# Kernel tuning notes

Measured on AMD Instinct MI355X. Metric: run time of the kernel, lower is better.

## Reference

```python
import jax, jax.numpy as jnp
import numpy as np

N_NODES = 8192


def spmm(edge_src, edge_dst, edge_w, h):
    # out[dst] += w * h[src]  — sparse adjacency @ dense matrix
    msg = h[edge_src] * edge_w[:, None]
    return jax.ops.segment_sum(msg, edge_dst, num_segments=N_NODES)


def setup_inputs() -> dict:
    key = jax.random.key(0)
    k_x, k_s, k_d, k_w, k_w1, k_w2 = jax.random.split(key, 6)
    x = jax.random.normal(k_x, (N_NODES, 512), dtype=jnp.float32)
    edge_src = jax.random.randint(k_s, (262144,), 0, N_NODES, dtype=jnp.int32)
    edge_dst = jax.random.randint(k_d, (262144,), 0, N_NODES, dtype=jnp.int32)
    edge_w = jax.random.uniform(k_w, (262144,), dtype=jnp.float32)
    W1 = jax.random.normal(k_w1, (512, 256), dtype=jnp.float32) * 0.05
    W2 = jax.random.normal(k_w2, (256, 64), dtype=jnp.float32) * 0.05
    return {"x": x, "edge_src": edge_src, "edge_dst": edge_dst,
            "edge_w": edge_w, "W1": W1, "W2": W2}


def reference(x, edge_src, edge_dst, edge_w, W1, W2):
    # GCN layer 1: relu(A @ (X W1))
    h1 = jax.nn.relu(spmm(edge_src, edge_dst, edge_w, x @ W1))
    # GCN layer 2 (linear act): Z = A @ (H1 W2)
    z = spmm(edge_src, edge_dst, edge_w, h1 @ W2)
    # InnerProductDecoder with identity act: Z @ Z^T
    recon = jnp.einsum('nd,md->nm', z, z)
    return recon
```

## Files before the change

kernel.cpp:

```cpp
#include <hip/hip_runtime.h>
#include <hip/hip_bf16.h>

#define NN     8192
#define D0     512
#define D1     256
#define D2     64
#define NE     262144

typedef __attribute__((ext_vector_type(8)))  __bf16 bf16x8;
typedef __attribute__((ext_vector_type(16))) float  f32x16;

__global__ __launch_bounds__(256) void prep_k(const float* __restrict__ W,
                                              int4* __restrict__ zero_region,
                                              __bf16* __restrict__ Th,
                                              __bf16* __restrict__ Tl) {
    const int bid = blockIdx.x;
    const int tid = threadIdx.x;
    if (bid < 16) {
        zero_region[bid * 256 + tid] = make_int4(0, 0, 0, 0);
    } else {
        __shared__ float t[32][33];
        const int cid = bid - 16;
        const int c0 = (cid & 7) * 32;
        const int k0 = (cid >> 3) * 32;
        {
            int tr  = tid >> 3;
            int tc4 = tid & 7;
            float4 v = *reinterpret_cast<const float4*>(&W[(k0 + tr) * D1 + c0 + tc4 * 4]);
            t[tr][tc4 * 4 + 0] = v.x;
            t[tr][tc4 * 4 + 1] = v.y;
            t[tr][tc4 * 4 + 2] = v.z;
            t[tr][tc4 * 4 + 3] = v.w;
        }
        __syncthreads();
        int c  = tid >> 3;
        int kq = (tid & 7) * 4;
        __bf16 hv[4], lv[4];
        #pragma unroll
        for (int j = 0; j < 4; ++j) {
            float f = t[kq + j][c];
            hv[j] = (__bf16)f;
            lv[j] = (__bf16)(f - (float)hv[j]);
        }
        *reinterpret_cast<uint2*>(&Th[(size_t)(c0 + c) * D0 + k0 + kq]) = *reinterpret_cast<uint2*>(hv);
        *reinterpret_cast<uint2*>(&Tl[(size_t)(c0 + c) * D0 + k0 + kq]) = *reinterpret_cast<uint2*>(lv);
    }
}

__global__ __launch_bounds__(256) void gemm1hist_k(const float* __restrict__ X,
                                                   const __bf16* __restrict__ Wh,
                                                   const __bf16* __restrict__ Wl,
                                                   float* __restrict__ O,
                                                   const int4* __restrict__ dst4,
                                                   int* __restrict__ counts) {
    const int gid = blockIdx.x;
    const int tid = threadIdx.x;
    if (gid >= 128) {
        int i = (gid - 128) * 256 + tid;
        int4 d = dst4[i];
        atomicAdd(&counts[d.x], 1);
        atomicAdd(&counts[d.y], 1);
        atomicAdd(&counts[d.z], 1);
        atomicAdd(&counts[d.w], 1);
        return;
    }
    const int bx = gid >> 1;
    const int by = gid & 1;
    const int lane = tid & 63;
    const int w    = tid >> 6;
    const int wm   = w >> 1;
    const int wn   = w & 1;
    const int r32  = lane & 31;
    const int kh   = lane >> 5;
    const int rowBase = bx * 128 + wm * 64;
    const int colBase = by * 128 + wn * 64;

    f32x16 acc[2][2] = {};

    for (int k0 = 0; k0 < D0; k0 += 16) {
        const int koff = k0 + kh * 8;
        bf16x8 ah[2], al[2];
        #pragma unroll
        for (int i = 0; i < 2; ++i) {
            const float* px = X + (size_t)(rowBase + i * 32 + r32) * D0 + koff;
            float4 f0 = *reinterpret_cast<const float4*>(px);
            float4 f1 = *reinterpret_cast<const float4*>(px + 4);
            float f[8] = {f0.x, f0.y, f0.z, f0.w, f1.x, f1.y, f1.z, f1.w};
            #pragma unroll
            for (int e = 0; e < 8; ++e) {
                __bf16 hj = (__bf16)f[e];
                ah[i][e] = hj;
                al[i][e] = (__bf16)(f[e] - (float)hj);
            }
        }
        bf16x8 bh[2], bl[2];
        #pragma unroll
        for (int j = 0; j < 2; ++j) {
            bh[j] = *reinterpret_cast<const bf16x8*>(Wh + (size_t)(colBase + j * 32 + r32) * D0 + koff);
            bl[j] = *reinterpret_cast<const bf16x8*>(Wl + (size_t)(colBase + j * 32 + r32) * D0 + koff);
        }
        #pragma unroll
        for (int i = 0; i < 2; ++i)
            #pragma unroll
            for (int j = 0; j < 2; ++j) {
                acc[i][j] = __builtin_amdgcn_mfma_f32_32x32x16_bf16(ah[i], bh[j], acc[i][j], 0, 0, 0);
                acc[i][j] = __builtin_amdgcn_mfma_f32_32x32x16_bf16(ah[i], bl[j], acc[i][j], 0, 0, 0);
                acc[i][j] = __builtin_amdgcn_mfma_f32_32x32x16_bf16(al[i], bh[j], acc[i][j], 0, 0, 0);
            }
    }

    #pragma unroll
    for (int i = 0; i < 2; ++i)
        #pragma unroll
        for (int j = 0; j < 2; ++j)
            #pragma unroll
            for (int reg = 0; reg < 16; ++reg) {
                int r = (reg & 3) + 8 * (reg >> 2) + 4 * kh;
                O[(size_t)(rowBase + i * 32 + r) * D1 + colBase + j * 32 + r32] = acc[i][j][reg];
            }
}

__global__ __launch_bounds__(256) void scan_k(const int* __restrict__ counts,
                                              int* __restrict__ rs) {
    __shared__ int wsum[4];
    const int tid  = threadIdx.x;
    const int base = tid * 32;
    int v[32];
    int s = 0;
    #pragma unroll
    for (int j = 0; j < 8; ++j) {
        int4 q = reinterpret_cast<const int4*>(&counts[base])[j];
        v[j * 4 + 0] = q.x; v[j * 4 + 1] = q.y; v[j * 4 + 2] = q.z; v[j * 4 + 3] = q.w;
        s += q.x + q.y + q.z + q.w;
    }
    int inc = s;
    #pragma unroll
    for (int off = 1; off < 64; off <<= 1) {
        int t = __shfl_up(inc, off, 64);
        if ((tid & 63) >= off) inc += t;
    }
    if ((tid & 63) == 63) wsum[tid >> 6] = inc;
    __syncthreads();
    int wpre = 0;
    #pragma unroll
    for (int wi = 0; wi < 4; ++wi) if (wi < (tid >> 6)) wpre += wsum[wi];
    int ex = wpre + inc - s;
    #pragma unroll
    for (int j = 0; j < 32; ++j) { rs[base + j] = ex; ex += v[j]; }
    if (tid == 0) rs[NN] = NE;
}

__global__ __launch_bounds__(256) void scatter_k(const int4* __restrict__ src4,
                                                 const int4* __restrict__ dst4,
                                                 const float4* __restrict__ w4,
                                                 const int* __restrict__ rs,
                                                 int* __restrict__ cursor,
                                                 int* __restrict__ eps,
                                                 float* __restrict__ epw) {
    int i = blockIdx.x * 256 + threadIdx.x;
    int4   s = src4[i];
    int4   d = dst4[i];
    float4 w = w4[i];
    int p;
    p = rs[d.x] + atomicAdd(&cursor[d.x], 1); eps[p] = s.x; epw[p] = w.x;
    p = rs[d.y] + atomicAdd(&cursor[d.y], 1); eps[p] = s.y; epw[p] = w.y;
    p = rs[d.z] + atomicAdd(&cursor[d.z], 1); eps[p] = s.z; epw[p] = w.z;
    p = rs[d.w] + atomicAdd(&cursor[d.w], 1); eps[p] = s.w; epw[p] = w.w;
}

__global__ __launch_bounds__(256) void spmmfuse_k(const float* __restrict__ Hin,
                                                  const int* __restrict__ rs,
                                                  const int* __restrict__ eps,
                                                  const float* __restrict__ epw,
                                                  const float* __restrict__ W2,
                                                  float* __restrict__ H1W2) {
    __shared__ float h1row[4][D1];
    const int tid = threadIdx.x;
    const int g   = tid >> 6;
    const int lc  = (tid & 63) * 4;
    const int row = blockIdx.x * 4 + g;
    const int start = rs[row], end = rs[row + 1];
    float4 acc = make_float4(0.f, 0.f, 0.f, 0.f);
    for (int j = start; j < end; ++j) {
        const float w = epw[j];
        float4 v = *reinterpret_cast<const float4*>(&Hin[(size_t)eps[j] * D1 + lc]);
        acc.x += w * v.x; acc.y += w * v.y; acc.z += w * v.z; acc.w += w * v.w;
    }
    h1row[g][lc + 0] = fmaxf(acc.x, 0.f);
    h1row[g][lc + 1] = fmaxf(acc.y, 0.f);
    h1row[g][lc + 2] = fmaxf(acc.z, 0.f);
    h1row[g][lc + 3] = fmaxf(acc.w, 0.f);
    __syncthreads();
    const int c = tid & 63;
    float o = 0.f;
    #pragma unroll 16
    for (int k = 0; k < D1; ++k) o += h1row[g][k] * W2[k * D2 + c];
    H1W2[(size_t)row * D2 + c] = o;
}

__global__ __launch_bounds__(256) void spmm64_k(const float* __restrict__ Hin,
                                                const int* __restrict__ rs,
                                                const int* __restrict__ eps,
                                                const float* __restrict__ epw,
                                                __bf16* __restrict__ Zh,
                                                __bf16* __restrict__ Zl) {
    const int tid = threadIdx.x;
    const int g   = tid >> 4;
    const int lc  = (tid & 15) * 4;
    const int row = blockIdx.x * 16 + g;
    const int start = rs[row], end = rs[row + 1];
    float4 acc = make_float4(0.f, 0.f, 0.f, 0.f);
    for (int j = start; j < end; ++j) {
        const float w = epw[j];
        float4 v = *reinterpret_cast<const float4*>(&Hin[(size_t)eps[j] * D2 + lc]);
        acc.x += w * v.x; acc.y += w * v.y; acc.z += w * v.z; acc.w += w * v.w;
    }
    float a[4] = {acc.x, acc.y, acc.z, acc.w};
    __bf16 h4[4], l4[4];
    #pragma unroll
    for (int e = 0; e < 4; ++e) {
        __bf16 h = (__bf16)a[e];
        h4[e] = h;
        l4[e] = (__bf16)(a[e] - (float)h);
    }
    *reinterpret_cast<uint2*>(&Zh[(size_t)row * D2 + lc]) = *reinterpret_cast<uint2*>(h4);
    *reinterpret_cast<uint2*>(&Zl[(size_t)row * D2 + lc]) = *reinterpret_cast<uint2*>(l4);
}

__global__ __launch_bounds__(256) void zzt_k(const __bf16* __restrict__ Zh,
                                             const __bf16* __restrict__ Zl,
                                             float* __restrict__ O) {
    const int tid  = threadIdx.x;
    const int lane = tid & 63;
    const int w    = tid >> 6;
    const int wm   = w >> 1;
    const int wn   = w & 1;
    const int r32  = lane & 31;
    const int kh   = lane >> 5;
    const int rowBase = blockIdx.y * 128 + wm * 64;
    const int colBase = blockIdx.x * 128 + wn * 64;

    f32x16 acc[2][2] = {};

    #pragma unroll
    for (int kk = 0; kk < 4; ++kk) {
        const int koff = kk * 16 + kh * 8;
        bf16x8 ah0 = *reinterpret_cast<const bf16x8*>(&Zh[(rowBase +      r32) * D2 + koff]);
        bf16x8 ah1 = *reinterpret_cast<const bf16x8*>(&Zh[(rowBase + 32 + r32) * D2 + koff]);
        bf16x8 al0 = *reinterpret_cast<const bf16x8*>(&Zl[(rowBase +      r32) * D2 + koff]);
        bf16x8 al1 = *reinterpret_cast<const bf16x8*>(&Zl[(rowBase + 32 + r32) * D2 + koff]);
        bf16x8 bh0 = *reinterpret_cast<const bf16x8*>(&Zh[(colBase +      r32) * D2 + koff]);
        bf16x8 bh1 = *reinterpret_cast<const bf16x8*>(&Zh[(colBase + 32 + r32) * D2 + koff]);
        bf16x8 bl0 = *reinterpret_cast<const bf16x8*>(&Zl[(colBase +      r32) * D2 + koff]);
        bf16x8 bl1 = *reinterpret_cast<const bf16x8*>(&Zl[(colBase + 32 + r32) * D2 + koff]);

        acc[0][0] = __builtin_amdgcn_mfma_f32_32x32x16_bf16(ah0, bh0, acc[0][0], 0, 0, 0);
        acc[0][1] = __builtin_amdgcn_mfma_f32_32x32x16_bf16(ah0, bh1, acc[0][1], 0, 0, 0);
        acc[1][0] = __builtin_amdgcn_mfma_f32_32x32x16_bf16(ah1, bh0, acc[1][0], 0, 0, 0);
        acc[1][1] = __builtin_amdgcn_mfma_f32_32x32x16_bf16(ah1, bh1, acc[1][1], 0, 0, 0);

        acc[0][0] = __builtin_amdgcn_mfma_f32_32x32x16_bf16(ah0, bl0, acc[0][0], 0, 0, 0);
        acc[0][1] = __builtin_amdgcn_mfma_f32_32x32x16_bf16(ah0, bl1, acc[0][1], 0, 0, 0);
        acc[1][0] = __builtin_amdgcn_mfma_f32_32x32x16_bf16(ah1, bl0, acc[1][0], 0, 0, 0);
        acc[1][1] = __builtin_amdgcn_mfma_f32_32x32x16_bf16(ah1, bl1, acc[1][1], 0, 0, 0);

        acc[0][0] = __builtin_amdgcn_mfma_f32_32x32x16_bf16(al0, bh0, acc[0][0], 0, 0, 0);
        acc[0][1] = __builtin_amdgcn_mfma_f32_32x32x16_bf16(al0, bh1, acc[0][1], 0, 0, 0);
        acc[1][0] = __builtin_amdgcn_mfma_f32_32x32x16_bf16(al1, bh0, acc[1][0], 0, 0, 0);
        acc[1][1] = __builtin_amdgcn_mfma_f32_32x32x16_bf16(al1, bh1, acc[1][1], 0, 0, 0);
    }

    #pragma unroll
    for (int i = 0; i < 2; ++i)
        #pragma unroll
        for (int j = 0; j < 2; ++j)
            #pragma unroll
            for (int reg = 0; reg < 16; ++reg) {
                int r = (reg & 3) + 8 * (reg >> 2) + 4 * kh;
                __builtin_nontemporal_store(acc[i][j][reg],
                    &O[(size_t)(rowBase + i * 32 + r) * NN + colBase + j * 32 + r32]);
            }
}

extern "C" void kernel_launch(void* const* d_in, const int* in_sizes, int n_in,
                              void* d_out, int out_size, void* d_ws, size_t ws_size,
                              hipStream_t stream) {
    const float* x        = (const float*)d_in[0];
    const int*   edge_src = (const int*)d_in[1];
    const int*   edge_dst = (const int*)d_in[2];
    const float* edge_w   = (const float*)d_in[3];
    const float* W1       = (const float*)d_in[4];
    const float* W2       = (const float*)d_in[5];
    float* out = (float*)d_out;

    char* ws = (char*)d_ws;
    const size_t OFF_XW1  = 0;
    const size_t OFF_H1W2 = OFF_XW1  + (size_t)NN * D1 * 4;
    const size_t OFF_ZH   = OFF_H1W2 + (size_t)NN * D2 * 4;
    const size_t OFF_ZL   = OFF_ZH   + (size_t)NN * D2 * 2;
    const size_t OFF_WTH  = OFF_ZL   + (size_t)NN * D2 * 2;
    const size_t OFF_WTL  = OFF_WTH  + (size_t)D0 * D1 * 2;
    const size_t OFF_RS   = OFF_WTL  + (size_t)D0 * D1 * 2;
    const size_t OFF_CNT  = OFF_RS   + 33280;
    const size_t OFF_CUR  = OFF_CNT  + (size_t)NN * 4;
    const size_t OFF_EPS  = OFF_CUR  + (size_t)NN * 4;
    const size_t OFF_EPW  = OFF_EPS  + (size_t)NE * 4;

    float*  xw1  = (float*)(ws + OFF_XW1);
    float*  h1w2 = (float*)(ws + OFF_H1W2);
    __bf16* zh   = (__bf16*)(ws + OFF_ZH);
    __bf16* zl   = (__bf16*)(ws + OFF_ZL);
    __bf16* wth  = (__bf16*)(ws + OFF_WTH);
    __bf16* wtl  = (__bf16*)(ws + OFF_WTL);
    int*    rs   = (int*)(ws + OFF_RS);
    int*    cnt  = (int*)(ws + OFF_CNT);
    int*    cur  = (int*)(ws + OFF_CUR);
    int*    eps  = (int*)(ws + OFF_EPS);
    float*  epw  = (float*)(ws + OFF_EPW);

    prep_k<<<16 + 128, 256, 0, stream>>>(W1, (int4*)cnt, wth, wtl);

    gemm1hist_k<<<128 + 256, 256, 0, stream>>>(x, wth, wtl, xw1,
                                               (const int4*)edge_dst, cnt);

    scan_k<<<1, 256, 0, stream>>>(cnt, rs);
    scatter_k<<<NE / 4 / 256, 256, 0, stream>>>((const int4*)edge_src,
                                                (const int4*)edge_dst,
                                                (const float4*)edge_w,
                                                rs, cur, eps, epw);

    spmmfuse_k<<<NN / 4, 256, 0, stream>>>(xw1, rs, eps, epw, W2, h1w2);

    spmm64_k<<<NN / 16, 256, 0, stream>>>(h1w2, rs, eps, epw, zh, zl);

    zzt_k<<<dim3(NN / 128, NN / 128), 256, 0, stream>>>(zh, zl, out);
}
```

Measured before the change: 211.1 us.

## Shrink GEMM1 tiles, pack edge index/weight pairs, split SpMM1 from GEMM2

GEMM1 now uses 64x64 block tiles with one 32x32 MFMA tile per wave, giving 512 blocks instead of 128 for more parallelism on the GPU. Edge source index and weight are packed into one int2 array so each edge needs one load instead of two. The fused SpMM1+W2 kernel is split into a column-split SpMM kernel (two column halves, 8 rows per block) and a separate small GEMM2 kernel. The split adds an extra pass that writes and reads the full H1 buffer through memory and an additional launch. It also gives up the register-level reuse of X and W tiles that the larger GEMM1 tiles had.

```diff
diff --git a/kernel.cpp b/kernel.cpp
--- a/kernel.cpp
+++ b/kernel.cpp
@@ -55,8 +55,8 @@
                                                    int* __restrict__ counts) {
     const int gid = blockIdx.x;
     const int tid = threadIdx.x;
-    if (gid >= 128) {
-        int i = (gid - 128) * 256 + tid;
+    if (gid >= 512) {
+        int i = (gid - 512) * 256 + tid;
         int4 d = dst4[i];
         atomicAdd(&counts[d.x], 1);
         atomicAdd(&counts[d.y], 1);
@@ -64,60 +64,49 @@
         atomicAdd(&counts[d.w], 1);
         return;
     }
-    const int bx = gid >> 1;
-    const int by = gid & 1;
+    const int bx = gid >> 2;
+    const int by = gid & 3;
     const int lane = tid & 63;
     const int w    = tid >> 6;
     const int wm   = w >> 1;
     const int wn   = w & 1;
     const int r32  = lane & 31;
     const int kh   = lane >> 5;
-    const int rowBase = bx * 128 + wm * 64;
-    const int colBase = by * 128 + wn * 64;
-
-    f32x16 acc[2][2] = {};
-
+    const int row  = bx * 64 + wm * 32 + r32;
+    const int col  = by * 64 + wn * 32 + r32;
+
+    const float*  pX  = X  + (size_t)row * D0;
+    const __bf16* pBh = Wh + (size_t)col * D0;
+    const __bf16* pBl = Wl + (size_t)col * D0;
+
+    f32x16 acc = {};
+    #pragma unroll 4
     for (int k0 = 0; k0 < D0; k0 += 16) {
         const int koff = k0 + kh * 8;
-        bf16x8 ah[2], al[2];
+        float4 f0 = *reinterpret_cast<const float4*>(pX + koff);
+        float4 f1 = *reinterpret_cast<const float4*>(pX + koff + 4);
+        float f[8] = {f0.x, f0.y, f0.z, f0.w, f1.x, f1.y, f1.z, f1.w};
+        bf16x8 ah, al;
         #pragma unroll
-        for (int i = 0; i < 2; ++i) {
-            const float* px = X + (size_t)(rowBase + i * 32 + r32) * D0 + koff;
-            float4 f0 = *reinterpret_cast<const float4*>(px);
-            float4 f1 = *reinterpret_cast<const float4*>(px + 4);
-            float f[8] = {f0.x, f0.y, f0.z, f0.w, f1.x, f1.y, f1.z, f1.w};
-            #pragma unroll
-            for (int e = 0; e < 8; ++e) {
-                __bf16 hj = (__bf16)f[e];
-                ah[i][e] = hj;
-                al[i][e] = (__bf16)(f[e] - (float)hj);
-            }
+        for (int e = 0; e < 8; ++e) {
+            __bf16 hj = (__bf16)f[e];
+            ah[e] = hj;
+            al[e] = (__bf16)(f[e] - (float)hj);
         }
-        bf16x8 bh[2], bl[2];
-        #pragma unroll
-        for (int j = 0; j < 2; ++j) {
-            bh[j] = *reinterpret_cast<const bf16x8*>(Wh + (size_t)(colBase + j * 32 + r32) * D0 + koff);
-            bl[j] = *reinterpret_cast<const bf16x8*>(Wl + (size_t)(colBase + j * 32 + r32) * D0 + koff);
-        }
-        #pragma unroll
-        for (int i = 0; i < 2; ++i)
-            #pragma unroll
-            for (int j = 0; j < 2; ++j) {
-                acc[i][j] = __builtin_amdgcn_mfma_f32_32x32x16_bf16(ah[i], bh[j], acc[i][j], 0, 0, 0);
-                acc[i][j] = __builtin_amdgcn_mfma_f32_32x32x16_bf16(ah[i], bl[j], acc[i][j], 0, 0, 0);
-                acc[i][j] = __builtin_amdgcn_mfma_f32_32x32x16_bf16(al[i], bh[j], acc[i][j], 0, 0, 0);
-            }
-    }
-
-    #pragma unroll
-    for (int i = 0; i < 2; ++i)
-        #pragma unroll
-        for (int j = 0; j < 2; ++j)
-            #pragma unroll
-            for (int reg = 0; reg < 16; ++reg) {
-                int r = (reg & 3) + 8 * (reg >> 2) + 4 * kh;
-                O[(size_t)(rowBase + i * 32 + r) * D1 + colBase + j * 32 + r32] = acc[i][j][reg];
-            }
+        bf16x8 bh = *reinterpret_cast<const bf16x8*>(pBh + koff);
+        bf16x8 bl = *reinterpret_cast<const bf16x8*>(pBl + koff);
+        acc = __builtin_amdgcn_mfma_f32_32x32x16_bf16(ah, bh, acc, 0, 0, 0);
+        acc = __builtin_amdgcn_mfma_f32_32x32x16_bf16(ah, bl, acc, 0, 0, 0);
+        acc = __builtin_amdgcn_mfma_f32_32x32x16_bf16(al, bh, acc, 0, 0, 0);
+    }
+
+    const int rowBase = bx * 64 + wm * 32;
+    const int colBase = by * 64 + wn * 32;
+    #pragma unroll
+    for (int reg = 0; reg < 16; ++reg) {
+        int r = (reg & 3) + 8 * (reg >> 2) + 4 * kh;
+        O[(size_t)(rowBase + r) * D1 + colBase + r32] = acc[reg];
+    }
 }
 
 __global__ __launch_bounds__(256) void scan_k(const int* __restrict__ counts,
@@ -155,53 +144,62 @@
                                                  const float4* __restrict__ w4,
                                                  const int* __restrict__ rs,
                                                  int* __restrict__ cursor,
-                                                 int* __restrict__ eps,
-                                                 float* __restrict__ epw) {
+                                                 int2* __restrict__ ep) {
     int i = blockIdx.x * 256 + threadIdx.x;
     int4   s = src4[i];
     int4   d = dst4[i];
     float4 w = w4[i];
     int p;
-    p = rs[d.x] + atomicAdd(&cursor[d.x], 1); eps[p] = s.x; epw[p] = w.x;
-    p = rs[d.y] + atomicAdd(&cursor[d.y], 1); eps[p] = s.y; epw[p] = w.y;
-    p = rs[d.z] + atomicAdd(&cursor[d.z], 1); eps[p] = s.z; epw[p] = w.z;
-    p = rs[d.w] + atomicAdd(&cursor[d.w], 1); eps[p] = s.w; epw[p] = w.w;
-}
-
-__global__ __launch_bounds__(256) void spmmfuse_k(const float* __restrict__ Hin,
-                                                  const int* __restrict__ rs,
-                                                  const int* __restrict__ eps,
-                                                  const float* __restrict__ epw,
-                                                  const float* __restrict__ W2,
-                                                  float* __restrict__ H1W2) {
-    __shared__ float h1row[4][D1];
-    const int tid = threadIdx.x;
-    const int g   = tid >> 6;
-    const int lc  = (tid & 63) * 4;
-    const int row = blockIdx.x * 4 + g;
+    p = rs[d.x] + atomicAdd(&cursor[d.x], 1); ep[p] = make_int2(s.x, __float_as_int(w.x));
+    p = rs[d.y] + atomicAdd(&cursor[d.y], 1); ep[p] = make_int2(s.y, __float_as_int(w.y));
+    p = rs[d.z] + atomicAdd(&cursor[d.z], 1); ep[p] = make_int2(s.z, __float_as_int(w.z));
+    p = rs[d.w] + atomicAdd(&cursor[d.w], 1); ep[p] = make_int2(s.w, __float_as_int(w.w));
+}
+
+__global__ __launch_bounds__(256) void spmm1_k(const float* __restrict__ Hin,
+                                               const int* __restrict__ rs,
+                                               const int2* __restrict__ ep,
+                                               float* __restrict__ H1) {
+    const int tid = threadIdx.x;
+    const int g   = tid >> 5;
+    const int lc  = blockIdx.y * 128 + (tid & 31) * 4;
+    const int row = blockIdx.x * 8 + g;
     const int start = rs[row], end = rs[row + 1];
     float4 acc = make_float4(0.f, 0.f, 0.f, 0.f);
     for (int j = start; j < end; ++j) {
-        const float w = epw[j];
-        float4 v = *reinterpret_cast<const float4*>(&Hin[(size_t)eps[j] * D1 + lc]);
+        int2 e = ep[j];
+        const float w = __int_as_float(e.y);
+        float4 v = *reinterpret_cast<const float4*>(&Hin[(size_t)e.x * D1 + lc]);
         acc.x += w * v.x; acc.y += w * v.y; acc.z += w * v.z; acc.w += w * v.w;
     }
-    h1row[g][lc + 0] = fmaxf(acc.x, 0.f);
-    h1row[g][lc + 1] = fmaxf(acc.y, 0.f);
-    h1row[g][lc + 2] = fmaxf(acc.z, 0.f);
-    h1row[g][lc + 3] = fmaxf(acc.w, 0.f);
+    float4 r = make_float4(fmaxf(acc.x, 0.f), fmaxf(acc.y, 0.f),
+                           fmaxf(acc.z, 0.f), fmaxf(acc.w, 0.f));
+    *reinterpret_cast<float4*>(&H1[(size_t)row * D1 + lc]) = r;
+}
+
+__global__ __launch_bounds__(256) void gemm2_k(const float* __restrict__ H,
+                                               const float* __restrict__ W,
+                                               float* __restrict__ O) {
+    __shared__ __align__(16) float hs[4][D1];
+    const int tid = threadIdx.x;
+    const int r = tid >> 6;
+    const int c = tid & 63;
+    const int row0 = blockIdx.x * 4;
+    {
+        int lr = tid >> 6, lc4 = tid & 63;
+        *reinterpret_cast<float4*>(&hs[lr][lc4 * 4]) =
+            *reinterpret_cast<const float4*>(&H[(size_t)(row0 + lr) * D1 + lc4 * 4]);
+    }
     __syncthreads();
-    const int c = tid & 63;
-    float o = 0.f;
+    float acc = 0.f;
     #pragma unroll 16
-    for (int k = 0; k < D1; ++k) o += h1row[g][k] * W2[k * D2 + c];
-    H1W2[(size_t)row * D2 + c] = o;
+    for (int k = 0; k < D1; ++k) acc += hs[r][k] * W[k * D2 + c];
+    O[(size_t)(row0 + r) * D2 + c] = acc;
 }
 
 __global__ __launch_bounds__(256) void spmm64_k(const float* __restrict__ Hin,
                                                 const int* __restrict__ rs,
-                                                const int* __restrict__ eps,
-                                                const float* __restrict__ epw,
+                                                const int2* __restrict__ ep,
                                                 __bf16* __restrict__ Zh,
                                                 __bf16* __restrict__ Zl) {
     const int tid = threadIdx.x;
@@ -211,8 +209,9 @@
     const int start = rs[row], end = rs[row + 1];
     float4 acc = make_float4(0.f, 0.f, 0.f, 0.f);
     for (int j = start; j < end; ++j) {
-        const float w = epw[j];
-        float4 v = *reinterpret_cast<const float4*>(&Hin[(size_t)eps[j] * D2 + lc]);
+        int2 e = ep[j];
+        const float w = __int_as_float(e.y);
+        float4 v = *reinterpret_cast<const float4*>(&Hin[(size_t)e.x * D2 + lc]);
         acc.x += w * v.x; acc.y += w * v.y; acc.z += w * v.z; acc.w += w * v.w;
     }
     float a[4] = {acc.x, acc.y, acc.z, acc.w};
@@ -295,7 +294,8 @@
 
     char* ws = (char*)d_ws;
     const size_t OFF_XW1  = 0;
-    const size_t OFF_H1W2 = OFF_XW1  + (size_t)NN * D1 * 4;
+    const size_t OFF_H1   = OFF_XW1  + (size_t)NN * D1 * 4;
+    const size_t OFF_H1W2 = OFF_H1   + (size_t)NN * D1 * 4;
     const size_t OFF_ZH   = OFF_H1W2 + (size_t)NN * D2 * 4;
     const size_t OFF_ZL   = OFF_ZH   + (size_t)NN * D2 * 2;
     const size_t OFF_WTH  = OFF_ZL   + (size_t)NN * D2 * 2;
@@ -303,10 +303,10 @@
     const size_t OFF_RS   = OFF_WTL  + (size_t)D0 * D1 * 2;
     const size_t OFF_CNT  = OFF_RS   + 33280;
     const size_t OFF_CUR  = OFF_CNT  + (size_t)NN * 4;
-    const size_t OFF_EPS  = OFF_CUR  + (size_t)NN * 4;
-    const size_t OFF_EPW  = OFF_EPS  + (size_t)NE * 4;
+    const size_t OFF_EP   = OFF_CUR  + (size_t)NN * 4;
 
     float*  xw1  = (float*)(ws + OFF_XW1);
+    float*  h1   = (float*)(ws + OFF_H1);
     float*  h1w2 = (float*)(ws + OFF_H1W2);
     __bf16* zh   = (__bf16*)(ws + OFF_ZH);
     __bf16* zl   = (__bf16*)(ws + OFF_ZL);
@@ -315,23 +315,24 @@
     int*    rs   = (int*)(ws + OFF_RS);
     int*    cnt  = (int*)(ws + OFF_CNT);
     int*    cur  = (int*)(ws + OFF_CUR);
-    int*    eps  = (int*)(ws + OFF_EPS);
-    float*  epw  = (float*)(ws + OFF_EPW);
+    int2*   ep   = (int2*)(ws + OFF_EP);
 
     prep_k<<<16 + 128, 256, 0, stream>>>(W1, (int4*)cnt, wth, wtl);
 
-    gemm1hist_k<<<128 + 256, 256, 0, stream>>>(x, wth, wtl, xw1,
+    gemm1hist_k<<<512 + 256, 256, 0, stream>>>(x, wth, wtl, xw1,
                                                (const int4*)edge_dst, cnt);
 
     scan_k<<<1, 256, 0, stream>>>(cnt, rs);
     scatter_k<<<NE / 4 / 256, 256, 0, stream>>>((const int4*)edge_src,
                                                 (const int4*)edge_dst,
                                                 (const float4*)edge_w,
-                                                rs, cur, eps, epw);
-
-    spmmfuse_k<<<NN / 4, 256, 0, stream>>>(xw1, rs, eps, epw, W2, h1w2);
-
-    spmm64_k<<<NN / 16, 256, 0, stream>>>(h1w2, rs, eps, epw, zh, zl);
+                                                rs, cur, ep);
+
+    spmm1_k<<<dim3(NN / 8, 2), 256, 0, stream>>>(xw1, rs, ep, h1);
+
+    gemm2_k<<<NN / 4, 256, 0, stream>>>(h1, W2, h1w2);
+
+    spmm64_k<<<NN / 16, 256, 0, stream>>>(h1w2, rs, ep, zh, zl);
 
     zzt_k<<<dim3(NN / 128, NN / 128), 256, 0, stream>>>(zh, zl, out);
 }
```

After: 218.4 us. 1.03x slower.
